# Kernel optimization log

Measured on AMD Instinct MI355X. Metric: run time of the kernel, lower is better.

Reference implementation:

```python
import jax, jax.numpy as jnp
import numpy as np

B, S, D, H = 32, 578, 1024, 16  # seq = (384//16)**2 + 2 = 578
DH = D // H  # 64, per-head size
INIT_STD = 0.02


def setup_inputs() -> dict:
    key = jax.random.key(0)
    ks = jax.random.split(key, 7)
    hidden_states = jax.random.normal(ks[0], (B, S, D), dtype=jnp.float32)
    # Per-head Dense layers: stack H separate [D, DH] kernels -> [H, D, DH]
    Wq = jax.random.normal(ks[1], (H, D, DH), dtype=jnp.float32) * INIT_STD
    Wk = jax.random.normal(ks[2], (H, D, DH), dtype=jnp.float32) * INIT_STD
    Wv = jax.random.normal(ks[3], (H, D, DH), dtype=jnp.float32) * INIT_STD
    bq = jax.random.normal(ks[4], (H, DH), dtype=jnp.float32) * INIT_STD
    bk = jax.random.normal(ks[5], (H, DH), dtype=jnp.float32) * INIT_STD
    bv = jax.random.normal(ks[6], (H, DH), dtype=jnp.float32) * INIT_STD
    return {"hidden_states": hidden_states, "Wq": Wq, "bq": bq,
            "Wk": Wk, "bk": bk, "Wv": Wv, "bv": bv}


def reference(hidden_states, Wq, bq, Wk, bk, Wv, bv):
    # Per-head Dense projections (original: Python list of H Dense layers),
    # expressed as one batched einsum over the head axis.
    # hidden_states: [B, S, D]; W*: [H, D, E]; b*: [H, E]
    q = jnp.einsum('bsd,hde->bhse', hidden_states, Wq) + bq[None, :, None, :]
    k = jnp.einsum('bsd,hde->bhse', hidden_states, Wk) + bk[None, :, None, :]
    v = jnp.einsum('bsd,hde->bhse', hidden_states, Wv) + bv[None, :, None, :]
    scale = 1.0 / jnp.sqrt(jnp.asarray(DH, dtype=q.dtype))
    scores = jnp.einsum('bhse,bhte->bhst', q, k) * scale  # [B, H, S, S]
    probs = jax.nn.softmax(scores, axis=-1)  # stable_softmax; dropout p=0
    out = jnp.einsum('bhst,bhte->bhse', probs, v)  # [B, H, S, E]
    # concat heads along last axis -> [B, S, H*E]
    return out.transpose(0, 2, 1, 3).reshape(B, S, H * DH)
```

## Files before the change

### kernel.cpp

```cpp
#include <hip/hip_runtime.h>

typedef __attribute__((ext_vector_type(8))) short short8;
typedef __attribute__((ext_vector_type(4))) float f32x4;
typedef unsigned short u16;
typedef unsigned int u32;

#define B_ 32
#define S_ 578
#define D_ 1024
#define H_ 16
#define DH_ 64
#define M_ 18496
#define MP_ 18560
#define N_ 3072
#define K_ 1024
#define ST_ 640
#define BHROWS_ (B_ * H_ * S_ + 64)
#define SCALE2 0.18033688011112042f
#define CMAX 16.0f

__device__ __forceinline__ u16 f2bf(float x) {
  u32 u = __float_as_uint(x);
  u = (u + 0x7fffu + ((u >> 16) & 1u)) >> 16;
  return (u16)u;
}

__device__ __forceinline__ void gload_lds16(const u16* g, u16* l) {
  __builtin_amdgcn_global_load_lds((const __attribute__((address_space(1))) void*)g,
                                   (__attribute__((address_space(3))) void*)l, 16, 0, 0);
}

__global__ __launch_bounds__(256) void cvt_hidden(const float* __restrict__ in, u16* __restrict__ o) {
  long i = ((long)blockIdx.x * 256 + threadIdx.x) * 8;
  float4 f0 = *(const float4*)(in + i);
  float4 f1 = *(const float4*)(in + i + 4);
  short8 v;
  u16* p = (u16*)&v;
  p[0] = f2bf(f0.x); p[1] = f2bf(f0.y); p[2] = f2bf(f0.z); p[3] = f2bf(f0.w);
  p[4] = f2bf(f1.x); p[5] = f2bf(f1.y); p[6] = f2bf(f1.z); p[7] = f2bf(f1.w);
  *(short8*)(o + i) = v;
}

__global__ __launch_bounds__(256) void wt_kernel(const float* __restrict__ Wq, const float* __restrict__ Wk,
                                                 const float* __restrict__ Wv, u16* __restrict__ Wt) {
  const int d0 = blockIdx.x * 64;
  const int h = blockIdx.y;
  const int qkv = blockIdx.z;
  const float* W = (qkv == 0) ? Wq : ((qkv == 1) ? Wk : Wv);
  __shared__ float tile[64][65];
  const int t = threadIdx.x;
  {
    int e = t & 63, dr = t >> 6;
#pragma unroll
    for (int p = 0; p < 16; ++p) {
      int dd = dr + p * 4;
      tile[dd][e] = W[((long)h * D_ + d0 + dd) * DH_ + e];
    }
  }
  __syncthreads();
  {
    int dd = t & 63, er = t >> 6;
#pragma unroll
    for (int p = 0; p < 16; ++p) {
      int ee = er + p * 4;
      long n = (long)qkv * 1024 + h * 64 + ee;
      Wt[n * K_ + d0 + dd] = f2bf(tile[dd][ee]);
    }
  }
}

__global__ __launch_bounds__(256) void bias_kernel(const float* __restrict__ bq, const float* __restrict__ bk,
                                                   const float* __restrict__ bv, float* __restrict__ bias) {
  int i = blockIdx.x * 256 + threadIdx.x;
  if (i < 3072) {
    const float* src = (i < 1024) ? bq : ((i < 2048) ? bk : bv);
    bias[i] = src[i & 1023];
  }
}

__global__ __launch_bounds__(256) void qkv_gemm(const u16* __restrict__ A, const u16* __restrict__ Bt,
                                                const float* __restrict__ bias,
                                                u16* __restrict__ qb, u16* __restrict__ kb, u16* __restrict__ vbt) {
  __shared__ alignas(16) u16 As[128 * 32];
  __shared__ alignas(16) u16 Bs[128 * 32];
  const int tid = threadIdx.x, wave = tid >> 6, lane = tid & 63, quad = lane >> 4, l16 = lane & 15;
  const long m0 = (long)blockIdx.x * 128, n0 = (long)blockIdx.y * 128;
  const u16* Ag = A + m0 * K_;
  const u16* Bg = Bt + n0 * K_;

  f32x4 acc[4][4];
#pragma unroll
  for (int mi = 0; mi < 4; ++mi)
#pragma unroll
    for (int ni = 0; ni < 4; ++ni) { f32x4 z = {0.f, 0.f, 0.f, 0.f}; acc[mi][ni] = z; }

  const int srow = lane >> 2;
  const int gchunk = (lane & 3) ^ ((lane >> 3) & 3);
  const int scol = gchunk * 8;
  const int r0 = 32 * wave;
  const int sw = quad ^ ((l16 >> 1) & 3);
  const int rb = (wave >> 1) * 64 + l16;
  const int cb = (wave & 1) * 64 + l16;

  for (int it = 0; it < 32; ++it) {
    const int k0 = it * 32;
    gload_lds16(Ag + (long)(r0 + srow) * K_ + k0 + scol,      &As[r0 * 32 + lane * 8]);
    gload_lds16(Ag + (long)(r0 + 16 + srow) * K_ + k0 + scol, &As[(r0 + 16) * 32 + lane * 8]);
    gload_lds16(Bg + (long)(r0 + srow) * K_ + k0 + scol,      &Bs[r0 * 32 + lane * 8]);
    gload_lds16(Bg + (long)(r0 + 16 + srow) * K_ + k0 + scol, &Bs[(r0 + 16) * 32 + lane * 8]);
    __syncthreads();
    const short8* Asv = (const short8*)As;
    const short8* Bsv = (const short8*)Bs;
    short8 a[4], b2[4];
#pragma unroll
    for (int mi = 0; mi < 4; ++mi) a[mi] = Asv[(rb + mi * 16) * 4 + sw];
#pragma unroll
    for (int ni = 0; ni < 4; ++ni) b2[ni] = Bsv[(cb + ni * 16) * 4 + sw];
#pragma unroll
    for (int mi = 0; mi < 4; ++mi)
#pragma unroll
      for (int ni = 0; ni < 4; ++ni)
        acc[mi][ni] = __builtin_amdgcn_mfma_f32_16x16x32_bf16(a[mi], b2[ni], acc[mi][ni], 0, 0, 0);
    __syncthreads();
  }

  float bv4[4]; int hh[4], ee[4];
#pragma unroll
  for (int ni = 0; ni < 4; ++ni) {
    long n = n0 + (wave & 1) * 64 + ni * 16 + l16;
    bv4[ni] = bias[n];
    hh[ni] = (int)((n >> 6) & 15);
    ee[ni] = (int)(n & 63);
  }
  const int qkv = (int)(n0 >> 10);
  if (qkv == 2) {
#pragma unroll
    for (int mi = 0; mi < 4; ++mi) {
#pragma unroll
      for (int r = 0; r < 4; ++r) {
        long m = m0 + (wave >> 1) * 64 + mi * 16 + quad * 4 + r;
        if (m < M_) {
          unsigned bi = (unsigned)m / (unsigned)S_;
          unsigned si = (unsigned)m - bi * (unsigned)S_;
#pragma unroll
          for (int ni = 0; ni < 4; ++ni) {
            float v = acc[mi][ni][r] + bv4[ni];
            vbt[((long)(bi * H_ + hh[ni]) * DH_ + ee[ni]) * ST_ + si] = f2bf(v);
          }
        }
      }
    }
  } else {
    u16* dst = (qkv == 0) ? qb : kb;
#pragma unroll
    for (int mi = 0; mi < 4; ++mi) {
#pragma unroll
      for (int r = 0; r < 4; ++r) {
        long m = m0 + (wave >> 1) * 64 + mi * 16 + quad * 4 + r;
        if (m < M_) {
          unsigned bi = (unsigned)m / (unsigned)S_;
          unsigned si = (unsigned)m - bi * (unsigned)S_;
          long rowb = ((long)bi * H_) * S_ * DH_ + (long)si * DH_;
#pragma unroll
          for (int ni = 0; ni < 4; ++ni) {
            float v = acc[mi][ni][r] + bv4[ni];
            dst[rowb + (long)hh[ni] * (S_ * DH_) + ee[ni]] = f2bf(v);
          }
        }
      }
    }
  }
}

__global__ __launch_bounds__(256) void attn_kernel(const u16* __restrict__ qb, const u16* __restrict__ kb,
                                                   const u16* __restrict__ vbt, float* __restrict__ out) {
  __shared__ alignas(16) u16 Ks[64 * 64];
  __shared__ alignas(16) u16 Vs[64 * 64];
  __shared__ alignas(16) u16 Ps[4 * 16 * 72];
  const int tid = threadIdx.x, wave = tid >> 6, lane = tid & 63, quad = lane >> 4, l16 = lane & 15;
  const int qt = blockIdx.x, h = blockIdx.y, b = blockIdx.z;
  const long bh = (long)b * H_ + h;
  const u16* qp = qb + bh * S_ * DH_;
  const u16* kp = kb + bh * S_ * DH_;
  const u16* vtp = vbt + bh * DH_ * ST_;
  const int q0 = qt * 64;

  short8 qf0, qf1;
  {
    int row = q0 + wave * 16 + l16;
    const short8* qv = (const short8*)(qp + (long)row * DH_);
    qf0 = qv[quad];
    qf1 = qv[4 + quad];
  }

  f32x4 O[4];
#pragma unroll
  for (int et = 0; et < 4; ++et) { f32x4 z = {0.f, 0.f, 0.f, 0.f}; O[et] = z; }
  float lp[4] = {0.f, 0.f, 0.f, 0.f};

  const int srow0 = tid >> 3;
  const int slot = tid & 7;
  const int s0 = quad ^ (l16 & 7);

  for (int kt = 0; kt < 10; ++kt) {
    const int t0 = kt * 64;
    __syncthreads();
#pragma unroll
    for (int p = 0; p < 2; ++p) {
      int row = srow0 + 32 * p;
      int gch = slot ^ (row & 7);
      gload_lds16(kp + (long)(t0 + row) * DH_ + gch * 8, &Ks[(tid + 256 * p) * 8]);
      gload_lds16(vtp + (long)row * ST_ + t0 + gch * 8, &Vs[(tid + 256 * p) * 8]);
    }
    __syncthreads();

    float p[4][4];
    const short8* Kv8 = (const short8*)Ks;
#pragma unroll
    for (int jt = 0; jt < 4; ++jt) {
      f32x4 sacc = {0.f, 0.f, 0.f, 0.f};
      short8 kf0 = Kv8[(16 * jt + l16) * 8 + s0];
      short8 kf1 = Kv8[(16 * jt + l16) * 8 + ((quad + 4) ^ (l16 & 7))];
      sacc = __builtin_amdgcn_mfma_f32_16x16x32_bf16(qf0, kf0, sacc, 0, 0, 0);
      sacc = __builtin_amdgcn_mfma_f32_16x16x32_bf16(qf1, kf1, sacc, 0, 0, 0);
      bool valid = (t0 + 16 * jt + l16) < S_;
#pragma unroll
      for (int r = 0; r < 4; ++r) {
        float e = valid ? exp2f(sacc[r] * SCALE2 - CMAX) : 0.f;
        p[jt][r] = e;
        lp[r] += e;
      }
    }

    u16* Pw = Ps + wave * 16 * 72;
#pragma unroll
    for (int jt = 0; jt < 4; ++jt)
#pragma unroll
      for (int r = 0; r < 4; ++r)
        Pw[(quad * 4 + r) * 72 + 16 * jt + l16] = f2bf(p[jt][r]);

    const short8* Pv8 = (const short8*)(Ps + wave * 16 * 72);
    const short8* Vv8 = (const short8*)Vs;
#pragma unroll
    for (int ks = 0; ks < 2; ++ks) {
      short8 pa = Pv8[l16 * 9 + ks * 4 + quad];
#pragma unroll
      for (int et = 0; et < 4; ++et) {
        short8 vf = Vv8[(16 * et + l16) * 8 + ((ks * 4 + quad) ^ (l16 & 7))];
        O[et] = __builtin_amdgcn_mfma_f32_16x16x32_bf16(pa, vf, O[et], 0, 0, 0);
      }
    }
  }

  float inv[4];
#pragma unroll
  for (int r = 0; r < 4; ++r) {
    float s = lp[r];
    s += __shfl_xor(s, 1);
    s += __shfl_xor(s, 2);
    s += __shfl_xor(s, 4);
    s += __shfl_xor(s, 8);
    inv[r] = 1.0f / s;
  }
#pragma unroll
  for (int et = 0; et < 4; ++et)
#pragma unroll
    for (int r = 0; r < 4; ++r) {
      int s = q0 + wave * 16 + quad * 4 + r;
      if (s < S_) out[((long)b * S_ + s) * (H_ * DH_) + (long)h * DH_ + et * 16 + l16] = O[et][r] * inv[r];
    }
}

extern "C" void kernel_launch(void* const* d_in, const int* in_sizes, int n_in,
                              void* d_out, int out_size, void* d_ws, size_t ws_size,
                              hipStream_t stream) {
  const float* hs = (const float*)d_in[0];
  const float* Wq = (const float*)d_in[1];
  const float* bq = (const float*)d_in[2];
  const float* Wk = (const float*)d_in[3];
  const float* bk = (const float*)d_in[4];
  const float* Wv = (const float*)d_in[5];
  const float* bv = (const float*)d_in[6];
  float* out = (float*)d_out;

  u16* Abf = (u16*)d_ws;
  u16* Wt = Abf + (size_t)MP_ * K_;
  float* bias = (float*)(Wt + (size_t)N_ * K_);
  u16* qb = (u16*)(bias + N_);
  u16* kb = qb + (size_t)BHROWS_ * DH_;
  u16* vbt = kb + (size_t)BHROWS_ * DH_;

  cvt_hidden<<<dim3(9248), dim3(256), 0, stream>>>(hs, Abf);
  wt_kernel<<<dim3(16, 16, 3), dim3(256), 0, stream>>>(Wq, Wk, Wv, Wt);
  bias_kernel<<<dim3(12), dim3(256), 0, stream>>>(bq, bk, bv, bias);
  qkv_gemm<<<dim3(145, 24), dim3(256), 0, stream>>>(Abf, Wt, bias, qb, kb, vbt);
  attn_kernel<<<dim3(10, 16, 32), dim3(256), 0, stream>>>(qb, kb, vbt, out);
}
```

Baseline: 483.4 us.

## Rewrite QKV GEMM with 256x256 tiles, triple-buffered LDS pipeline and XCD-aware mapping

Replaces the 128x128 single-buffered QKV projection GEMM with 256x256 tiles computed by 512-thread blocks. Global-to-LDS loads are triple-buffered and issued ahead, with explicit vmcnt waits, barriers and priority bumps so loads overlap the MFMA work. Workgroups are remapped so each XCD gets a contiguous chunk of tiles, and the padded A buffer is zero-filled to a multiple of 256 rows. The larger tile raises register and LDS use, and the padding adds wasted rows in the last M tile.

After: 454.7 us. -5.9%, faster.

```diff
diff --git a/kernel.cpp b/kernel.cpp
--- a/kernel.cpp
+++ b/kernel.cpp
@@ -11,7 +11,7 @@
 #define H_ 16
 #define DH_ 64
 #define M_ 18496
-#define MP_ 18560
+#define MP2_ 18688
 #define N_ 3072
 #define K_ 1024
 #define ST_ 640
@@ -32,6 +32,11 @@
 
 __global__ __launch_bounds__(256) void cvt_hidden(const float* __restrict__ in, u16* __restrict__ o) {
   long i = ((long)blockIdx.x * 256 + threadIdx.x) * 8;
+  if (i >= (long)M_ * D_) {
+    short8 z = {0, 0, 0, 0, 0, 0, 0, 0};
+    *(short8*)(o + i) = z;
+    return;
+  }
   float4 f0 = *(const float4*)(in + i);
   float4 f1 = *(const float4*)(in + i + 4);
   short8 v;
@@ -78,93 +83,141 @@
   }
 }
 
-__global__ __launch_bounds__(256) void qkv_gemm(const u16* __restrict__ A, const u16* __restrict__ Bt,
-                                                const float* __restrict__ bias,
-                                                u16* __restrict__ qb, u16* __restrict__ kb, u16* __restrict__ vbt) {
-  __shared__ alignas(16) u16 As[128 * 32];
-  __shared__ alignas(16) u16 Bs[128 * 32];
-  const int tid = threadIdx.x, wave = tid >> 6, lane = tid & 63, quad = lane >> 4, l16 = lane & 15;
-  const long m0 = (long)blockIdx.x * 128, n0 = (long)blockIdx.y * 128;
+
+__device__ __forceinline__ void stage256(const u16* __restrict__ g, u16* l, int tid, int k0) {
+  const int r = tid >> 2;
+  const int gch = (tid & 3) ^ ((tid >> 3) & 3);
+  const u16* src = g + (long)r * K_ + k0 + gch * 8;
+  gload_lds16(src, l + tid * 8);
+  gload_lds16(src + 128L * K_, l + 4096 + tid * 8);
+}
+
+template <int CUR, int NX2, bool STG, int VM>
+__device__ __forceinline__ void tile_step(const u16* __restrict__ Ag, const u16* __restrict__ Bg,
+                                          u16 (*Abuf)[256 * 32], u16 (*Bbuf)[256 * 32],
+                                          f32x4 (&acc)[8][4], int tid, int arow, int brow, int sw, int k2) {
+  const short8* Av = (const short8*)Abuf[CUR];
+  const short8* Bv = (const short8*)Bbuf[CUR];
+  if constexpr (STG) stage256(Ag, Abuf[NX2], tid, k2);
+  if constexpr (VM == 6) asm volatile("s_waitcnt vmcnt(6)" ::: "memory");
+  else if constexpr (VM == 4) asm volatile("s_waitcnt vmcnt(4)" ::: "memory");
+  else asm volatile("s_waitcnt vmcnt(0)" ::: "memory");
+  __builtin_amdgcn_s_barrier();
+  __builtin_amdgcn_sched_barrier(0);
+  short8 a[8], b0, b1;
+#pragma unroll
+  for (int mi = 0; mi < 8; ++mi) a[mi] = Av[(arow + mi * 16) * 4 + sw];
+  b0 = Bv[brow * 4 + sw];
+  b1 = Bv[(brow + 16) * 4 + sw];
+  asm volatile("s_waitcnt lgkmcnt(0)" ::: "memory");
+  __builtin_amdgcn_sched_barrier(0);
+  __builtin_amdgcn_s_setprio(1);
+#pragma unroll
+  for (int mi = 0; mi < 8; ++mi) {
+    acc[mi][0] = __builtin_amdgcn_mfma_f32_16x16x32_bf16(a[mi], b0, acc[mi][0], 0, 0, 0);
+    acc[mi][1] = __builtin_amdgcn_mfma_f32_16x16x32_bf16(a[mi], b1, acc[mi][1], 0, 0, 0);
+  }
+  __builtin_amdgcn_s_setprio(0);
+  __builtin_amdgcn_s_barrier();
+  __builtin_amdgcn_sched_barrier(0);
+  if constexpr (STG) stage256(Bg, Bbuf[NX2], tid, k2);
+  short8 b2 = Bv[(brow + 32) * 4 + sw];
+  short8 b3 = Bv[(brow + 48) * 4 + sw];
+  asm volatile("s_waitcnt lgkmcnt(0)" ::: "memory");
+  __builtin_amdgcn_sched_barrier(0);
+  __builtin_amdgcn_s_setprio(1);
+#pragma unroll
+  for (int mi = 0; mi < 8; ++mi) {
+    acc[mi][2] = __builtin_amdgcn_mfma_f32_16x16x32_bf16(a[mi], b2, acc[mi][2], 0, 0, 0);
+    acc[mi][3] = __builtin_amdgcn_mfma_f32_16x16x32_bf16(a[mi], b3, acc[mi][3], 0, 0, 0);
+  }
+  __builtin_amdgcn_s_setprio(0);
+  __builtin_amdgcn_s_barrier();
+  __builtin_amdgcn_sched_barrier(0);
+}
+
+__global__ __launch_bounds__(512, 2) void qkv_gemm(const u16* __restrict__ A, const u16* __restrict__ Bt,
+                                                   const float* __restrict__ bias,
+                                                   u16* __restrict__ qb, u16* __restrict__ kb,
+                                                   u16* __restrict__ vbt) {
+  __shared__ alignas(16) u16 Abuf[3][256 * 32];
+  __shared__ alignas(16) u16 Bbuf[3][256 * 32];
+  const int tid = threadIdx.x, wid = tid >> 6, lane = tid & 63, quad = lane >> 4, l16 = lane & 15;
+  const int wr = wid >> 2, wc = wid & 3;
+
+  const int nwg = 73 * 12;
+  const int qq = nwg >> 3, rr = nwg & 7;
+  int xcd = blockIdx.x & 7, loc = blockIdx.x >> 3;
+  int wg = (xcd < rr ? xcd * (qq + 1) : rr * (qq + 1) + (xcd - rr) * qq) + loc;
+  const int mt = wg / 12, nt = wg - mt * 12;
+  const long m0 = (long)mt * 256, n0 = (long)nt * 256;
   const u16* Ag = A + m0 * K_;
   const u16* Bg = Bt + n0 * K_;
 
-  f32x4 acc[4][4];
-#pragma unroll
-  for (int mi = 0; mi < 4; ++mi)
+  f32x4 acc[8][4];
+#pragma unroll
+  for (int mi = 0; mi < 8; ++mi)
 #pragma unroll
     for (int ni = 0; ni < 4; ++ni) { f32x4 z = {0.f, 0.f, 0.f, 0.f}; acc[mi][ni] = z; }
 
-  const int srow = lane >> 2;
-  const int gchunk = (lane & 3) ^ ((lane >> 3) & 3);
-  const int scol = gchunk * 8;
-  const int r0 = 32 * wave;
   const int sw = quad ^ ((l16 >> 1) & 3);
-  const int rb = (wave >> 1) * 64 + l16;
-  const int cb = (wave & 1) * 64 + l16;
-
-  for (int it = 0; it < 32; ++it) {
-    const int k0 = it * 32;
-    gload_lds16(Ag + (long)(r0 + srow) * K_ + k0 + scol,      &As[r0 * 32 + lane * 8]);
-    gload_lds16(Ag + (long)(r0 + 16 + srow) * K_ + k0 + scol, &As[(r0 + 16) * 32 + lane * 8]);
-    gload_lds16(Bg + (long)(r0 + srow) * K_ + k0 + scol,      &Bs[r0 * 32 + lane * 8]);
-    gload_lds16(Bg + (long)(r0 + 16 + srow) * K_ + k0 + scol, &Bs[(r0 + 16) * 32 + lane * 8]);
-    __syncthreads();
-    const short8* Asv = (const short8*)As;
-    const short8* Bsv = (const short8*)Bs;
-    short8 a[4], b2[4];
-#pragma unroll
-    for (int mi = 0; mi < 4; ++mi) a[mi] = Asv[(rb + mi * 16) * 4 + sw];
-#pragma unroll
-    for (int ni = 0; ni < 4; ++ni) b2[ni] = Bsv[(cb + ni * 16) * 4 + sw];
-#pragma unroll
-    for (int mi = 0; mi < 4; ++mi)
-#pragma unroll
-      for (int ni = 0; ni < 4; ++ni)
-        acc[mi][ni] = __builtin_amdgcn_mfma_f32_16x16x32_bf16(a[mi], b2[ni], acc[mi][ni], 0, 0, 0);
-    __syncthreads();
-  }
-
-  float bv4[4]; int hh[4], ee[4];
-#pragma unroll
-  for (int ni = 0; ni < 4; ++ni) {
-    long n = n0 + (wave & 1) * 64 + ni * 16 + l16;
-    bv4[ni] = bias[n];
-    hh[ni] = (int)((n >> 6) & 15);
-    ee[ni] = (int)(n & 63);
-  }
-  const int qkv = (int)(n0 >> 10);
-  if (qkv == 2) {
-#pragma unroll
-    for (int mi = 0; mi < 4; ++mi) {
+  const int arow = wr * 128 + l16;
+  const int brow = wc * 64 + l16;
+
+  stage256(Ag, Abuf[0], tid, 0);
+  stage256(Bg, Bbuf[0], tid, 0);
+  stage256(Ag, Abuf[1], tid, 32);
+  stage256(Bg, Bbuf[1], tid, 32);
+
+#pragma unroll 1
+  for (int t = 0; t < 30; t += 3) {
+    tile_step<0, 2, true, 6>(Ag, Bg, Abuf, Bbuf, acc, tid, arow, brow, sw, (t + 2) * 32);
+    tile_step<1, 0, true, 6>(Ag, Bg, Abuf, Bbuf, acc, tid, arow, brow, sw, (t + 3) * 32);
+    tile_step<2, 1, true, 6>(Ag, Bg, Abuf, Bbuf, acc, tid, arow, brow, sw, (t + 4) * 32);
+  }
+  tile_step<0, 2, false, 4>(Ag, Bg, Abuf, Bbuf, acc, tid, arow, brow, sw, 0);
+  tile_step<1, 0, false, 0>(Ag, Bg, Abuf, Bbuf, acc, tid, arow, brow, sw, 0);
+
+  const long nb = n0 + wc * 64;
+  const int h = (int)((nb >> 6) & 15);
+  const int qkvsel = (int)(nb >> 10);
+  float bv4[4];
+#pragma unroll
+  for (int ni = 0; ni < 4; ++ni) bv4[ni] = bias[nb + ni * 16 + l16];
+
+  if (qkvsel == 2) {
+#pragma unroll
+    for (int mi = 0; mi < 8; ++mi) {
 #pragma unroll
       for (int r = 0; r < 4; ++r) {
-        long m = m0 + (wave >> 1) * 64 + mi * 16 + quad * 4 + r;
+        long m = m0 + wr * 128 + mi * 16 + quad * 4 + r;
         if (m < M_) {
           unsigned bi = (unsigned)m / (unsigned)S_;
           unsigned si = (unsigned)m - bi * (unsigned)S_;
+          long base = ((long)(bi * H_ + h) * DH_) * ST_ + si;
 #pragma unroll
           for (int ni = 0; ni < 4; ++ni) {
             float v = acc[mi][ni][r] + bv4[ni];
-            vbt[((long)(bi * H_ + hh[ni]) * DH_ + ee[ni]) * ST_ + si] = f2bf(v);
+            vbt[base + (long)(ni * 16 + l16) * ST_] = f2bf(v);
           }
         }
       }
     }
   } else {
-    u16* dst = (qkv == 0) ? qb : kb;
-#pragma unroll
-    for (int mi = 0; mi < 4; ++mi) {
+    u16* dst = (qkvsel == 0) ? qb : kb;
+#pragma unroll
+    for (int mi = 0; mi < 8; ++mi) {
 #pragma unroll
       for (int r = 0; r < 4; ++r) {
-        long m = m0 + (wave >> 1) * 64 + mi * 16 + quad * 4 + r;
+        long m = m0 + wr * 128 + mi * 16 + quad * 4 + r;
         if (m < M_) {
           unsigned bi = (unsigned)m / (unsigned)S_;
           unsigned si = (unsigned)m - bi * (unsigned)S_;
-          long rowb = ((long)bi * H_) * S_ * DH_ + (long)si * DH_;
+          long base = ((long)(bi * H_ + h) * S_ + si) * DH_;
 #pragma unroll
           for (int ni = 0; ni < 4; ++ni) {
             float v = acc[mi][ni][r] + bv4[ni];
-            dst[rowb + (long)hh[ni] * (S_ * DH_) + ee[ni]] = f2bf(v);
+            dst[base + ni * 16 + l16] = f2bf(v);
           }
         }
       }
@@ -284,15 +337,15 @@
   float* out = (float*)d_out;
 
   u16* Abf = (u16*)d_ws;
-  u16* Wt = Abf + (size_t)MP_ * K_;
+  u16* Wt = Abf + (size_t)MP2_ * K_;
   float* bias = (float*)(Wt + (size_t)N_ * K_);
   u16* qb = (u16*)(bias + N_);
   u16* kb = qb + (size_t)BHROWS_ * DH_;
   u16* vbt = kb + (size_t)BHROWS_ * DH_;
 
-  cvt_hidden<<<dim3(9248), dim3(256), 0, stream>>>(hs, Abf);
+  cvt_hidden<<<dim3(9344), dim3(256), 0, stream>>>(hs, Abf);
   wt_kernel<<<dim3(16, 16, 3), dim3(256), 0, stream>>>(Wq, Wk, Wv, Wt);
   bias_kernel<<<dim3(12), dim3(256), 0, stream>>>(bq, bk, bv, bias);
-  qkv_gemm<<<dim3(145, 24), dim3(256), 0, stream>>>(Abf, Wt, bias, qb, kb, vbt);
+  qkv_gemm<<<dim3(876), dim3(512), 0, stream>>>(Abf, Wt, bias, qb, kb, vbt);
   attn_kernel<<<dim3(10, 16, 32), dim3(256), 0, stream>>>(qb, kb, vbt, out);
 }
```
